# Optimization experiments

Measured on AMD Instinct MI355X. Metric: run time of the kernel, lower is better.

Reference implementation:

```python
import jax, jax.numpy as jnp
import numpy as np

N = 10000   # nodes
B = 32      # batch (hardcoded in source)
E = 40000   # edges per graph
H = 4       # attention heads
D = 10      # out_feats per head (hardcoded 10 in source)
T = 10      # GAT input feature size (hardcoded 10)
L = 2       # n_align_layers
NEG = 0.2   # LeakyReLU slope


def _leaky(z):
    return jnp.where(z >= 0, z, NEG * z)


def _ln(t):
    # LayerNorm((N,B,D), elementwise_affine=False): normalize over the whole tensor
    m = t.mean()
    v = ((t - m) ** 2).mean()
    return (t - m) * jax.lax.rsqrt(v + 1e-5)


def _gat(feat, fc_w, a_l, a_r, src, dst):
    # feat: (N,B,T); fc_w: (H*D,T); a_l,a_r: (H,D); src,dst: (E,)
    ft = jnp.einsum('nbf,of->nbo', feat, fc_w).reshape(N, B, H, D)
    el = jnp.einsum('nbhd,hd->nbh', ft, a_l)   # (N,B,H)
    er = jnp.einsum('nbhd,hd->nbh', ft, a_r)
    e = _leaky(el[src] + er[dst])              # (E,B,H)
    emax = jax.ops.segment_max(e, dst, num_segments=N)
    ee = jnp.exp(e - emax[dst])
    a = ee / jax.ops.segment_sum(ee, dst, num_segments=N)[dst]  # edge softmax per dst
    out = jax.ops.segment_sum(ft[src] * a[..., None], dst, num_segments=N)  # (N,B,H,D)
    return _leaky(out)  # activation = leaky_relu in source


def setup_inputs():
    key = jax.random.key(0)
    ks = iter(jax.random.split(key, 40))
    x = jax.random.normal(next(ks), (T, N, B, 3), dtype=jnp.float32)
    idx = lambda: jax.random.randint(next(ks), (E,), 0, N, dtype=jnp.int32)
    inp = {'x': x, 'ps_src': idx(), 'ps_dst': idx(), 'rl_src': idx(), 'rl_dst': idx()}
    def gat_params(name):
        inp[name + '_fc'] = jax.random.normal(next(ks), (L, H * D, T), dtype=jnp.float32) * 0.3
        inp[name + '_al'] = jax.random.normal(next(ks), (L, H, D), dtype=jnp.float32) * 0.3
        inp[name + '_ar'] = jax.random.normal(next(ks), (L, H, D), dtype=jnp.float32) * 0.3
    for nm in ('mu_p', 'sg_p', 'mu_r', 'sg_r'):
        gat_params(nm)
    inp['reg_mu_w'] = jax.random.normal(next(ks), (1, T), dtype=jnp.float32) * 0.3
    inp['reg_mu_b'] = jnp.zeros((1,), dtype=jnp.float32)
    inp['reg_sg_w'] = jax.random.normal(next(ks), (1, T), dtype=jnp.float32) * 0.3
    inp['reg_sg_b'] = jnp.zeros((1,), dtype=jnp.float32)
    return inp


def reference(x, mu_p_fc, mu_p_al, mu_p_ar, sg_p_fc, sg_p_al, sg_p_ar,
              mu_r_fc, mu_r_al, mu_r_ar, sg_r_fc, sg_r_al, sg_r_ar,
              reg_mu_w, reg_mu_b, reg_sg_w, reg_sg_b,
              ps_src, ps_dst, rl_src, rl_dst):
    # mode='align1' path of Net.forward
    h = jnp.transpose(x, (1, 2, 0, 3))[..., :3]  # (N,B,T,3)
    mu = h[..., 0]      # (N,B,T)
    sigma = h[..., 1]
    mu_r0, sg_r0 = mu, sigma
    # pseudo-graph alignment stack
    mu_p, sg_p = mu, sigma
    for i in range(L - 1):
        mu_p = _ln(_gat(mu_p, mu_p_fc[i], mu_p_al[i], mu_p_ar[i], ps_src, ps_dst).mean(-2))
        sg_p = _ln(_gat(sg_p, sg_p_fc[i], sg_p_al[i], sg_p_ar[i], ps_src, ps_dst).mean(-2))
        h_p = (mu_p + sg_p) / 2
        mu_p, sg_p = h_p, h_p
    # real-graph alignment stack
    mu_rl, sg_rl = mu, sigma
    for i in range(L - 1):
        mu_rl = _ln(_gat(mu_rl, mu_r_fc[i], mu_r_al[i], mu_r_ar[i], rl_src, rl_dst).mean(-2))
        sg_rl = _ln(_gat(sg_rl, sg_r_fc[i], sg_r_al[i], sg_r_ar[i], rl_src, rl_dst).mean(-2))
        h_rl = (mu_rl + sg_rl) / 2
        mu_rl, sg_rl = h_rl, h_rl
    mu_r = mu_r0 @ reg_mu_w.T + reg_mu_b                                        # (N,B,1)
    mu_pf = _gat(h_p, mu_p_fc[-1], mu_p_al[-1], mu_p_ar[-1], ps_src, ps_dst).mean(-2)
    mu_rf = _gat(h_rl, mu_r_fc[-1], mu_r_al[-1], mu_r_ar[-1], rl_src, rl_dst).mean(-2)
    sg_r = sg_r0 @ reg_sg_w.T + reg_sg_b
    sg_pf = _gat(h_p, sg_p_fc[-1], sg_p_al[-1], sg_p_ar[-1], ps_src, ps_dst).mean(-2)
    sg_rf = _gat(h_rl, sg_r_fc[-1], sg_r_al[-1], sg_r_ar[-1], rl_src, rl_dst).mean(-2)
    return ((mu_r + mu_pf + mu_rf) / 3, (sg_r + sg_pf + sg_rf) / 3)
```

## Files before the change

kernel.cpp:

```cpp
#include <hip/hip_runtime.h>


#define NN 10000
#define BB 32
#define EE 40000
#define HH 4
#define DD 10
#define TT 10
#define FS 12
#define MS 24
#define NEG 0.2f

#define NB   (NN*BB)
#define NBT  (NN*BB*TT)
#define NBF  (NN*BB*FS)
#define NBM  (NN*BB*MS)

__global__ void extract_kernel(const float* __restrict__ x,
                               const float* __restrict__ wmu, const float* __restrict__ bmu,
                               const float* __restrict__ wsg, const float* __restrict__ bsg,
                               float* __restrict__ ms,
                               float* __restrict__ regmu, float* __restrict__ regsg) {
    int i = blockIdx.x * blockDim.x + threadIdx.x;
    if (i >= NB) return;
    int n = i / BB, b = i % BB;
    float smu = 0.f, ssg = 0.f;
    float muv[TT], sgv[TT];
#pragma unroll
    for (int t = 0; t < TT; t++) {
        size_t xi = (((size_t)t * NN + n) * BB + b) * 3;
        float m = x[xi], s = x[xi + 1];
        muv[t] = m; sgv[t] = s;
        smu += m * wmu[t];
        ssg += s * wsg[t];
    }
#pragma unroll
    for (int t = 0; t < TT; t++) {
        ms[(size_t)i * MS + t]      = muv[t];
        ms[(size_t)i * MS + 12 + t] = sgv[t];
    }
    regmu[i] = smu + bmu[0];
    regsg[i] = ssg + bsg[0];
}

__global__ void deg2_kernel(const int* __restrict__ dst0, int* __restrict__ deg0,
                            const int* __restrict__ dst1, int* __restrict__ deg1) {
    int e = blockIdx.x * blockDim.x + threadIdx.x;
    const int* dst = blockIdx.y ? dst1 : dst0;
    int* deg       = blockIdx.y ? deg1 : deg0;
    if (e < EE) atomicAdd(&deg[dst[e]], 1);
}

__global__ void scan2_kernel(const int* __restrict__ deg0, int* __restrict__ off0,
                             const int* __restrict__ deg1, int* __restrict__ off1) {
    const int* __restrict__ deg = blockIdx.x ? deg1 : deg0;
    int* __restrict__ off       = blockIdx.x ? off1 : off0;
    __shared__ int sm[16];
    __shared__ int carry_s;
    int tid = threadIdx.x;
    int lane = tid & 63, wid = tid >> 6;
    if (tid == 0) { carry_s = 0; off[0] = 0; }
    __syncthreads();
    for (int base = 0; base < NN; base += 1024) {
        int i = base + tid;
        int v = (i < NN) ? deg[i] : 0;
        int x = v;
#pragma unroll
        for (int s = 1; s < 64; s <<= 1) {
            int t = __shfl_up(x, s, 64);
            if (lane >= s) x += t;
        }
        if (lane == 63) sm[wid] = x;
        __syncthreads();
        if (wid == 0) {
            int w = (lane < 16) ? sm[lane] : 0;
#pragma unroll
            for (int s = 1; s < 16; s <<= 1) {
                int t = __shfl_up(w, s, 64);
                if (lane >= s) w += t;
            }
            if (lane < 16) sm[lane] = w;
        }
        __syncthreads();
        int add = carry_s + ((wid > 0) ? sm[wid - 1] : 0);
        if (i < NN) off[i + 1] = add + x;
        int total = sm[15];
        __syncthreads();
        if (tid == 0) carry_s += total;
        __syncthreads();
    }
}

__global__ void fill2_kernel(const int* __restrict__ src0, const int* __restrict__ dst0,
                             const int* __restrict__ off0, int* __restrict__ cur0,
                             int* __restrict__ csr0,
                             const int* __restrict__ src1, const int* __restrict__ dst1,
                             const int* __restrict__ off1, int* __restrict__ cur1,
                             int* __restrict__ csr1) {
    int e = blockIdx.x * blockDim.x + threadIdx.x;
    const int* src = blockIdx.y ? src1 : src0;
    const int* dst = blockIdx.y ? dst1 : dst0;
    const int* off = blockIdx.y ? off1 : off0;
    int* cursor    = blockIdx.y ? cur1 : cur0;
    int* csr       = blockIdx.y ? csr1 : csr0;
    if (e < EE) {
        int d = dst[e];
        int p = atomicAdd(&cursor[d], 1);
        csr[off[d] + p] = src[e];
    }
}

__global__ void hist2_kernel(const int* __restrict__ deg0, const int* __restrict__ deg1,
                             int* __restrict__ hist) {
    __shared__ int lh[64];
    if (threadIdx.x < 64) lh[threadIdx.x] = 0;
    __syncthreads();
    int n = blockIdx.x * blockDim.x + threadIdx.x;
    int g = blockIdx.y;
    const int* deg = g ? deg1 : deg0;
    if (n < NN) {
        int d = deg[n];
        int bin = 63 - ((d < 63) ? d : 63);
        atomicAdd(&lh[bin], 1);
    }
    __syncthreads();
    if (threadIdx.x < 64 && lh[threadIdx.x])
        atomicAdd(&hist[g * 64 + threadIdx.x], lh[threadIdx.x]);
}

__global__ void binoff_kernel(const int* __restrict__ hist, int* __restrict__ boff) {
    int g = threadIdx.x >> 6, lane = threadIdx.x & 63;
    int v = hist[g * 64 + lane];
    int x = v;
#pragma unroll
    for (int s = 1; s < 64; s <<= 1) {
        int t = __shfl_up(x, s, 64);
        if (lane >= s) x += t;
    }
    boff[g * 64 + lane] = x - v;
}

__global__ void permfill2_kernel(const int* __restrict__ deg0, const int* __restrict__ deg1,
                                 const int* __restrict__ boff, int* __restrict__ bcur,
                                 int* __restrict__ perm0, int* __restrict__ perm1) {
    __shared__ int lh[64], lbase[64];
    if (threadIdx.x < 64) lh[threadIdx.x] = 0;
    __syncthreads();
    int n = blockIdx.x * blockDim.x + threadIdx.x;
    int g = blockIdx.y;
    const int* deg = g ? deg1 : deg0;
    int* perm      = g ? perm1 : perm0;
    int bin = 0, myp = 0;
    if (n < NN) {
        int d = deg[n];
        bin = 63 - ((d < 63) ? d : 63);
        myp = atomicAdd(&lh[bin], 1);
    }
    __syncthreads();
    if (threadIdx.x < 64) {
        int c = lh[threadIdx.x];
        lbase[threadIdx.x] = c ? atomicAdd(&bcur[g * 64 + threadIdx.x], c) : 0;
    }
    __syncthreads();
    if (n < NN) perm[boff[g * 64 + bin] + lbase[bin] + myp] = n;
}

__global__ void vpre_kernel(const float* __restrict__ fc0, const float* __restrict__ al0, const float* __restrict__ ar0,
                            const float* __restrict__ fc1, const float* __restrict__ al1, const float* __restrict__ ar1,
                            const float* __restrict__ fc2, const float* __restrict__ al2, const float* __restrict__ ar2,
                            const float* __restrict__ fc3, const float* __restrict__ al3, const float* __restrict__ ar3,
                            float* __restrict__ vbuf) {
    int j = threadIdx.x;
    if (j >= 320) return;
    int g = j / 40, r = j % 40;
    int h = r / 10, t = r % 10;
    int which = g & 3, layer = g >> 2;
    const float* fc; const float* al; const float* ar;
    if (which == 0)      { fc = fc0; al = al0; ar = ar0; }
    else if (which == 1) { fc = fc1; al = al1; ar = ar1; }
    else if (which == 2) { fc = fc2; al = al2; ar = ar2; }
    else                 { fc = fc3; al = al3; ar = ar3; }
    fc += layer * (HH * DD * TT);
    al += layer * (HH * DD);
    ar += layer * (HH * DD);
    float vl = 0.f, vr = 0.f;
#pragma unroll
    for (int d = 0; d < DD; d++) {
        float w = fc[(h * DD + d) * TT + t];
        vl += al[h * DD + d] * w;
        vr += ar[h * DD + d] * w;
    }
    vbuf[g * 80 + r] = vl;
    vbuf[g * 80 + 40 + r] = vr;
}

struct PairCfg {
    const float* f;
    const float* WA; const float* WB;
    const float* vA; const float* vB;
    const int* off; const int* csr; const int* perm;
    float* gA; float* gB;
    float* statsA; float* statsB;
};
struct PairCfg2 { PairCfg c[2]; };

#define LOAD_ROW(dst, q)                                        \
    {                                                           \
        float4 _r0 = *(const float4*)(q);                       \
        float4 _r1 = *(const float4*)((q) + 4);                 \
        float2 _r2 = *(const float2*)((q) + 8);                 \
        dst[0]=_r0.x; dst[1]=_r0.y; dst[2]=_r0.z; dst[3]=_r0.w; \
        dst[4]=_r1.x; dst[5]=_r1.y; dst[6]=_r1.z; dst[7]=_r1.w; \
        dst[8]=_r2.x; dst[9]=_r2.y;                             \
    }

__device__ __forceinline__ void eacc(const float (&fa)[TT], bool val,
                                     const float* __restrict__ v,
                                     const float (&er)[HH],
                                     float (&den)[HH], float (&acc)[HH][TT]) {
#pragma unroll
    for (int h = 0; h < HH; h++) {
        float e = 0.f;
#pragma unroll
        for (int t = 0; t < TT; t++) e += v[h * TT + t] * fa[t];
        float z = e + er[h];
        z = (z >= 0.f) ? z : NEG * z;
        float w = val ? __expf(z) : 0.f;
        den[h] += w;
#pragma unroll
        for (int t = 0; t < TT; t++) acc[h][t] += w * fa[t];
    }
}

template <bool DUALF, bool STATS>
__global__ void __launch_bounds__(256)
gatpair_kernel(PairCfg2 cfgs) {
    const PairCfg cfg = cfgs.c[blockIdx.y];
    __shared__ __align__(16) float sWA[HH * DD * 12];
    __shared__ __align__(16) float sWB[HH * DD * 12];
    for (int kk = threadIdx.x; kk < HH * DD * TT; kk += blockDim.x) {
        int r = kk / TT, t = kk - r * TT;
        sWA[r * 12 + t] = cfg.WA[kk];
        sWB[r * 12 + t] = cfg.WB[kk];
    }
    __syncthreads();

    const float* __restrict__ f   = cfg.f;
    const int*   __restrict__ csr = cfg.csr;
    const float* __restrict__ vA  = cfg.vA;
    const float* __restrict__ vB  = cfg.vB;
    const int LDR = DUALF ? MS : FS;

    int i = blockIdx.x * blockDim.x + threadIdx.x;
    float lsA = 0.f, lqA = 0.f, lsB = 0.f, lqB = 0.f;
    if (i < NB) {
        int b = i & 31;
        int slot = i >> 5;
        int n = cfg.perm[slot];
        int nb = n * BB + b;
        int s0 = cfg.off[n], s1 = cfg.off[n + 1];

        float erA[HH], erB[HH];
        {
            const float* p = f + (size_t)nb * LDR;
            float fsA[TT];
            LOAD_ROW(fsA, p);
            float fsB[TT];
            if (DUALF) { LOAD_ROW(fsB, p + 12); }
#pragma unroll
            for (int h = 0; h < HH; h++) {
                float ea = 0.f, eb = 0.f;
#pragma unroll
                for (int t = 0; t < TT; t++) {
                    ea += vA[HH * TT + h * TT + t] * fsA[t];
                    eb += vB[HH * TT + h * TT + t] * (DUALF ? fsB[t] : fsA[t]);
                }
                erA[h] = ea; erB[h] = eb;
            }
        }

        float accA[HH][TT], accB[HH][TT];
        float denA[HH], denB[HH];
#pragma unroll
        for (int h = 0; h < HH; h++) {
            denA[h] = 0.f; denB[h] = 0.f;
#pragma unroll
            for (int t = 0; t < TT; t++) { accA[h][t] = 0.f; accB[h][t] = 0.f; }
        }

        for (int k = s0; k < s1; k += 2) {
            int k1 = (k + 1 < s1) ? k + 1 : k;
            bool v1 = (k + 1 < s1);
            int e0 = csr[k], e1 = csr[k1];
            const float* q0 = f + (size_t)(e0 * BB + b) * LDR;
            const float* q1 = f + (size_t)(e1 * BB + b) * LDR;
            float a0[TT], a1[TT];
            LOAD_ROW(a0, q0);
            LOAD_ROW(a1, q1);
            if (DUALF) {
                float b0[TT], b1[TT];
                LOAD_ROW(b0, q0 + 12);
                LOAD_ROW(b1, q1 + 12);
                eacc(a0, true, vA, erA, denA, accA);
                eacc(b0, true, vB, erB, denB, accB);
                eacc(a1, v1,   vA, erA, denA, accA);
                eacc(b1, v1,   vB, erB, denB, accB);
            } else {
                eacc(a0, true, vA, erA, denA, accA);
                eacc(a0, true, vB, erB, denB, accB);
                eacc(a1, v1,   vA, erA, denA, accA);
                eacc(a1, v1,   vB, erB, denB, accB);
            }
        }

        bool nz = (s1 > s0);
        float* gpA = cfg.gA + (size_t)nb * DD;
        float* gpB = cfg.gB + (size_t)nb * DD;

#pragma unroll
        for (int g = 0; g < 2; g++) {
            const float (*acc)[TT] = g ? accB : accA;
            const float* den = g ? denB : denA;
            const float* sW  = g ? sWB : sWA;
            float* gp        = g ? gpB : gpA;
            float rd[HH];
#pragma unroll
            for (int h = 0; h < HH; h++) rd[h] = nz ? (1.0f / den[h]) : 0.f;
            float outv[DD];
#pragma unroll
            for (int d = 0; d < DD; d++) outv[d] = 0.f;
#pragma unroll
            for (int h = 0; h < HH; h++) {
#pragma unroll
                for (int d = 0; d < DD; d++) {
                    const float* wr = &sW[(h * DD + d) * 12];
                    float4 w0 = *(const float4*)wr;
                    float4 w1 = *(const float4*)(wr + 4);
                    float2 w2 = *(const float2*)(wr + 8);
                    float va = w0.x * acc[h][0] + w0.y * acc[h][1] + w0.z * acc[h][2] + w0.w * acc[h][3]
                             + w1.x * acc[h][4] + w1.y * acc[h][5] + w1.z * acc[h][6] + w1.w * acc[h][7]
                             + w2.x * acc[h][8] + w2.y * acc[h][9];
                    va *= rd[h];
                    va = (va >= 0.f) ? va : NEG * va;
                    outv[d] += va * 0.25f;
                }
            }
#pragma unroll
            for (int d = 0; d < DD; d += 2)
                *(float2*)(gp + d) = make_float2(outv[d], outv[d + 1]);
            if (STATS) {
                float s = 0.f, q = 0.f;
#pragma unroll
                for (int d = 0; d < DD; d++) { s += outv[d]; q += outv[d] * outv[d]; }
                if (g) { lsB = s; lqB = q; } else { lsA = s; lqA = q; }
            }
        }
    }
    if (STATS) {
#pragma unroll
        for (int o = 32; o > 0; o >>= 1) {
            lsA += __shfl_down(lsA, o, 64);
            lqA += __shfl_down(lqA, o, 64);
            lsB += __shfl_down(lsB, o, 64);
            lqB += __shfl_down(lqB, o, 64);
        }
        __shared__ float ss[4][4];
        int wid = threadIdx.x >> 6, lid = threadIdx.x & 63;
        if (lid == 0) { ss[wid][0] = lsA; ss[wid][1] = lqA; ss[wid][2] = lsB; ss[wid][3] = lqB; }
        __syncthreads();
        if (threadIdx.x == 0) {
            float a0 = 0.f, a1 = 0.f, a2 = 0.f, a3 = 0.f;
#pragma unroll
            for (int w = 0; w < 4; w++) { a0 += ss[w][0]; a1 += ss[w][1]; a2 += ss[w][2]; a3 += ss[w][3]; }
            atomicAdd(&cfg.statsA[0], a0);
            atomicAdd(&cfg.statsA[1], a1);
            atomicAdd(&cfg.statsB[0], a2);
            atomicAdd(&cfg.statsB[1], a3);
        }
    }
}

__global__ void lncomb2_kernel(const float* __restrict__ gA, const float* __restrict__ gB,
                               const float* __restrict__ gA2, const float* __restrict__ gB2,
                               const float* __restrict__ stats,
                               float* __restrict__ hp, float* __restrict__ hrl) {
    int i = blockIdx.x * blockDim.x + threadIdx.x;
    if (i >= NBT) return;
    const float* ga = blockIdx.y ? gA2 : gA;
    const float* gb = blockIdx.y ? gB2 : gB;
    const float* st = stats + (blockIdx.y ? 4 : 0);
    float* h        = blockIdx.y ? hrl : hp;
    const float M = (float)NBT;
    float ma = st[0] / M; float va = st[1] / M - ma * ma;
    float mb = st[2] / M; float vb = st[3] / M - mb * mb;
    float ra = rsqrtf(va + 1e-5f), rb = rsqrtf(vb + 1e-5f);
    int nb = i / DD, t = i - nb * DD;
    h[(size_t)nb * FS + t] = 0.5f * ((ga[i] - ma) * ra + (gb[i] - mb) * rb);
}

__global__ void outcomb2_kernel(const float* __restrict__ regmu, const float* __restrict__ regsg,
                                const float* __restrict__ gA, const float* __restrict__ gA2,
                                const float* __restrict__ gB, const float* __restrict__ gB2,
                                float* __restrict__ out) {
    int i = blockIdx.x * blockDim.x + threadIdx.x;
    if (i >= NBT) return;
    int nb = i / DD;
    if (blockIdx.y == 0) out[i]       = (regmu[nb] + gA[i] + gA2[i]) * (1.0f / 3.0f);
    else                 out[NBT + i] = (regsg[nb] + gB[i] + gB2[i]) * (1.0f / 3.0f);
}

extern "C" void kernel_launch(void* const* d_in, const int* in_sizes, int n_in,
                              void* d_out, int out_size, void* d_ws, size_t ws_size,
                              hipStream_t stream) {
    const float* x      = (const float*)d_in[0];
    const int* ps_src   = (const int*)d_in[1];
    const int* ps_dst   = (const int*)d_in[2];
    const int* rl_src   = (const int*)d_in[3];
    const int* rl_dst   = (const int*)d_in[4];
    const float* mu_p_fc = (const float*)d_in[5];
    const float* mu_p_al = (const float*)d_in[6];
    const float* mu_p_ar = (const float*)d_in[7];
    const float* sg_p_fc = (const float*)d_in[8];
    const float* sg_p_al = (const float*)d_in[9];
    const float* sg_p_ar = (const float*)d_in[10];
    const float* mu_r_fc = (const float*)d_in[11];
    const float* mu_r_al = (const float*)d_in[12];
    const float* mu_r_ar = (const float*)d_in[13];
    const float* sg_r_fc = (const float*)d_in[14];
    const float* sg_r_al = (const float*)d_in[15];
    const float* sg_r_ar = (const float*)d_in[16];
    const float* reg_mu_w = (const float*)d_in[17];
    const float* reg_mu_b = (const float*)d_in[18];
    const float* reg_sg_w = (const float*)d_in[19];
    const float* reg_sg_b = (const float*)d_in[20];

    float* out = (float*)d_out;

    float* fw = (float*)d_ws;
    float* ms    = fw;              fw += NBM;
    float* hp    = fw;              fw += NBF;
    float* hrl   = fw;              fw += NBF;
    float* gA    = fw;              fw += NBT;
    float* gB    = fw;              fw += NBT;
    float* gA2   = fw;              fw += NBT;
    float* gB2   = fw;              fw += NBT;
    float* regmu = fw;              fw += NB;
    float* regsg = fw;              fw += NB;
    float* vbuf  = fw;              fw += 8 * 80;
    int* iw = (int*)fw;
    int* ps_off = iw;               iw += NN + 1;
    int* rl_off = iw;               iw += NN + 1;
    int* ps_csr = iw;               iw += EE;
    int* rl_csr = iw;               iw += EE;
    int* perm_ps = iw;              iw += NN;
    int* perm_rl = iw;              iw += NN;
    int* boff   = iw;               iw += 128;
    int* deg_ps = iw;               iw += NN;
    int* cur_ps = iw;               iw += NN;
    int* deg_rl = iw;               iw += NN;
    int* cur_rl = iw;               iw += NN;
    int* hist   = iw;               iw += 128;
    int* bcur   = iw;               iw += 128;
    float* stats = (float*)iw;
    size_t zero_bytes = (size_t)(4 * NN + 256) * sizeof(int) + 8 * sizeof(float);
    hipMemsetAsync(deg_ps, 0, zero_bytes, stream);

    const int TPB = 256;
    const int GRID_NB  = (NB + TPB - 1) / TPB;
    const int GRID_NBT = (NBT + TPB - 1) / TPB;
    const int GRID_E   = (EE + TPB - 1) / TPB;
    const int GRID_N   = (NN + TPB - 1) / TPB;

    extract_kernel<<<GRID_NB, TPB, 0, stream>>>(x, reg_mu_w, reg_mu_b, reg_sg_w, reg_sg_b,
                                                ms, regmu, regsg);

    {
        dim3 g(GRID_E, 2, 1);
        dim3 gn(GRID_N, 2, 1);
        deg2_kernel<<<g, TPB, 0, stream>>>(ps_dst, deg_ps, rl_dst, deg_rl);
        scan2_kernel<<<2, 1024, 0, stream>>>(deg_ps, ps_off, deg_rl, rl_off);
        fill2_kernel<<<g, TPB, 0, stream>>>(ps_src, ps_dst, ps_off, cur_ps, ps_csr,
                                            rl_src, rl_dst, rl_off, cur_rl, rl_csr);
        hist2_kernel<<<gn, TPB, 0, stream>>>(deg_ps, deg_rl, hist);
        binoff_kernel<<<1, 128, 0, stream>>>(hist, boff);
        permfill2_kernel<<<gn, TPB, 0, stream>>>(deg_ps, deg_rl, boff, bcur, perm_ps, perm_rl);
    }

    vpre_kernel<<<1, 320, 0, stream>>>(mu_p_fc, mu_p_al, mu_p_ar,
                                       sg_p_fc, sg_p_al, sg_p_ar,
                                       mu_r_fc, mu_r_al, mu_r_ar,
                                       sg_r_fc, sg_r_al, sg_r_ar, vbuf);

    {
        PairCfg2 c;
        c.c[0] = { ms, mu_p_fc, sg_p_fc, vbuf + 0 * 80, vbuf + 1 * 80,
                   ps_off, ps_csr, perm_ps, gA,  gB,  stats + 0, stats + 2 };
        c.c[1] = { ms, mu_r_fc, sg_r_fc, vbuf + 2 * 80, vbuf + 3 * 80,
                   rl_off, rl_csr, perm_rl, gA2, gB2, stats + 4, stats + 6 };
        dim3 grid(GRID_NB, 2, 1);
        gatpair_kernel<true, true><<<grid, TPB, 0, stream>>>(c);
    }
    {
        dim3 g(GRID_NBT, 2, 1);
        lncomb2_kernel<<<g, TPB, 0, stream>>>(gA, gB, gA2, gB2, stats, hp, hrl);
    }

    {
        PairCfg2 c;
        c.c[0] = { hp,  mu_p_fc + 400, sg_p_fc + 400, vbuf + 4 * 80, vbuf + 5 * 80,
                   ps_off, ps_csr, perm_ps, gA,  gB,  nullptr, nullptr };
        c.c[1] = { hrl, mu_r_fc + 400, sg_r_fc + 400, vbuf + 6 * 80, vbuf + 7 * 80,
                   rl_off, rl_csr, perm_rl, gA2, gB2, nullptr, nullptr };
        dim3 grid(GRID_NB, 2, 1);
        gatpair_kernel<false, false><<<grid, TPB, 0, stream>>>(c);
    }

    {
        dim3 g(GRID_NBT, 2, 1);
        outcomb2_kernel<<<g, TPB, 0, stream>>>(regmu, regsg, gA, gA2, gB, gB2, out);
    }
}
```

Baseline: 413.2 us.

## Split GAT feature rows across half-wavefronts with transposed 6-wide layout

Features are stored in a transposed layout where each node-batch row is split into two 6-float halves, so one 64-lane wavefront handles one destination node across all 32 batches and both halves. Per-edge attention logits and the final projections are completed with cross-half shuffles. The paired A/B GAT kernel becomes a single-GAT kernel launched over four configs, and the neighbour loads are software-prefetched one edge ahead. The intent is to halve per-thread register state and raise occupancy and load parallelism, at the cost of extra shuffles and of reading the shared input rows separately for each GAT.

Result: slower. 556.1 us (+34.6%).

```diff
diff --git a/kernel.cpp b/kernel.cpp
--- a/kernel.cpp
+++ b/kernel.cpp
@@ -8,24 +8,22 @@
 #define DD 10
 #define TT 10
 #define FS 12
-#define MS 24
 #define NEG 0.2f
 
 #define NB   (NN*BB)
 #define NBT  (NN*BB*TT)
 #define NBF  (NN*BB*FS)
-#define NBM  (NN*BB*MS)
 
 __global__ void extract_kernel(const float* __restrict__ x,
                                const float* __restrict__ wmu, const float* __restrict__ bmu,
                                const float* __restrict__ wsg, const float* __restrict__ bsg,
-                               float* __restrict__ ms,
+                               float* __restrict__ muT, float* __restrict__ sgT,
                                float* __restrict__ regmu, float* __restrict__ regsg) {
     int i = blockIdx.x * blockDim.x + threadIdx.x;
     if (i >= NB) return;
     int n = i / BB, b = i % BB;
     float smu = 0.f, ssg = 0.f;
-    float muv[TT], sgv[TT];
+    float muv[FS], sgv[FS];
 #pragma unroll
     for (int t = 0; t < TT; t++) {
         size_t xi = (((size_t)t * NN + n) * BB + b) * 3;
@@ -34,10 +32,13 @@
         smu += m * wmu[t];
         ssg += s * wsg[t];
     }
-#pragma unroll
-    for (int t = 0; t < TT; t++) {
-        ms[(size_t)i * MS + t]      = muv[t];
-        ms[(size_t)i * MS + 12 + t] = sgv[t];
+    muv[10] = 0.f; muv[11] = 0.f; sgv[10] = 0.f; sgv[11] = 0.f;
+#pragma unroll
+    for (int t = 0; t < FS; t++) {
+        int th = t / 6, j = t - th * 6;
+        size_t di = ((size_t)(n * 2 + th) * BB + b) * 6 + j;
+        muT[di] = muv[t];
+        sgT[di] = sgv[t];
     }
     regmu[i] = smu + bmu[0];
     regsg[i] = ssg + bsg[0];
@@ -194,188 +195,160 @@
     vbuf[g * 80 + 40 + r] = vr;
 }
 
-struct PairCfg {
+struct QCfg {
     const float* f;
-    const float* WA; const float* WB;
-    const float* vA; const float* vB;
+    const float* W;
+    const float* v;
     const int* off; const int* csr; const int* perm;
-    float* gA; float* gB;
-    float* statsA; float* statsB;
+    float* g; float* stats;
 };
-struct PairCfg2 { PairCfg c[2]; };
-
-#define LOAD_ROW(dst, q)                                        \
-    {                                                           \
-        float4 _r0 = *(const float4*)(q);                       \
-        float4 _r1 = *(const float4*)((q) + 4);                 \
-        float2 _r2 = *(const float2*)((q) + 8);                 \
-        dst[0]=_r0.x; dst[1]=_r0.y; dst[2]=_r0.z; dst[3]=_r0.w; \
-        dst[4]=_r1.x; dst[5]=_r1.y; dst[6]=_r1.z; dst[7]=_r1.w; \
-        dst[8]=_r2.x; dst[9]=_r2.y;                             \
-    }
-
-__device__ __forceinline__ void eacc(const float (&fa)[TT], bool val,
-                                     const float* __restrict__ v,
-                                     const float (&er)[HH],
-                                     float (&den)[HH], float (&acc)[HH][TT]) {
-#pragma unroll
-    for (int h = 0; h < HH; h++) {
-        float e = 0.f;
-#pragma unroll
-        for (int t = 0; t < TT; t++) e += v[h * TT + t] * fa[t];
-        float z = e + er[h];
-        z = (z >= 0.f) ? z : NEG * z;
-        float w = val ? __expf(z) : 0.f;
-        den[h] += w;
-#pragma unroll
-        for (int t = 0; t < TT; t++) acc[h][t] += w * fa[t];
-    }
-}
-
-template <bool DUALF, bool STATS>
+struct QCfg4 { QCfg c[4]; };
+
+template <bool STATS>
 __global__ void __launch_bounds__(256)
-gatpair_kernel(PairCfg2 cfgs) {
-    const PairCfg cfg = cfgs.c[blockIdx.y];
-    __shared__ __align__(16) float sWA[HH * DD * 12];
-    __shared__ __align__(16) float sWB[HH * DD * 12];
-    for (int kk = threadIdx.x; kk < HH * DD * TT; kk += blockDim.x) {
-        int r = kk / TT, t = kk - r * TT;
-        sWA[r * 12 + t] = cfg.WA[kk];
-        sWB[r * 12 + t] = cfg.WB[kk];
-    }
-    __syncthreads();
-
-    const float* __restrict__ f   = cfg.f;
-    const int*   __restrict__ csr = cfg.csr;
-    const float* __restrict__ vA  = cfg.vA;
-    const float* __restrict__ vB  = cfg.vB;
-    const int LDR = DUALF ? MS : FS;
-
-    int i = blockIdx.x * blockDim.x + threadIdx.x;
-    float lsA = 0.f, lqA = 0.f, lsB = 0.f, lqB = 0.f;
-    if (i < NB) {
-        int b = i & 31;
-        int slot = i >> 5;
+gatq_kernel(QCfg4 cfgs) {
+    const QCfg cfg = cfgs.c[blockIdx.y];
+    __shared__ __align__(16) float sW[HH * DD * 12];
+    __shared__ float svp[2 * HH * 12];
+    for (int kk = threadIdx.x; kk < HH * DD * 12; kk += blockDim.x) {
+        int r = kk / 12, t = kk - r * 12;
+        sW[kk] = (t < TT) ? cfg.W[r * TT + t] : 0.f;
+    }
+    if (threadIdx.x < 2 * HH * 12) {
+        int s = threadIdx.x / 48, r = threadIdx.x % 48;
+        int h = r / 12, t = r % 12;
+        svp[threadIdx.x] = (t < TT) ? cfg.v[s * 40 + h * TT + t] : 0.f;
+    }
+    __syncthreads();
+
+    int wid = threadIdx.x >> 6, lane = threadIdx.x & 63;
+    int th = lane >> 5, b = lane & 31;
+    int slot = blockIdx.x * 4 + wid;
+    float lsum = 0.f, lsq = 0.f;
+    if (slot < NN) {
         int n = cfg.perm[slot];
-        int nb = n * BB + b;
         int s0 = cfg.off[n], s1 = cfg.off[n + 1];
-
-        float erA[HH], erB[HH];
+        const float* __restrict__ f = cfg.f;
+        const int*   __restrict__ csr = cfg.csr;
+
+        float vl[HH][6];
+#pragma unroll
+        for (int h = 0; h < HH; h++)
+#pragma unroll
+            for (int j = 0; j < 6; j++) vl[h][j] = svp[h * 12 + th * 6 + j];
+
+        float er[HH];
         {
-            const float* p = f + (size_t)nb * LDR;
-            float fsA[TT];
-            LOAD_ROW(fsA, p);
-            float fsB[TT];
-            if (DUALF) { LOAD_ROW(fsB, p + 12); }
+            const float* p = f + ((size_t)n * 64 + lane) * 6;
+            float2 a = *(const float2*)p;
+            float2 c = *(const float2*)(p + 2);
+            float2 d = *(const float2*)(p + 4);
+            float fs[6] = {a.x, a.y, c.x, c.y, d.x, d.y};
 #pragma unroll
             for (int h = 0; h < HH; h++) {
-                float ea = 0.f, eb = 0.f;
-#pragma unroll
-                for (int t = 0; t < TT; t++) {
-                    ea += vA[HH * TT + h * TT + t] * fsA[t];
-                    eb += vB[HH * TT + h * TT + t] * (DUALF ? fsB[t] : fsA[t]);
-                }
-                erA[h] = ea; erB[h] = eb;
-            }
-        }
-
-        float accA[HH][TT], accB[HH][TT];
-        float denA[HH], denB[HH];
+                float e = 0.f;
+#pragma unroll
+                for (int j = 0; j < 6; j++) e += svp[48 + h * 12 + th * 6 + j] * fs[j];
+                e += __shfl_xor(e, 32, 64);
+                er[h] = e;
+            }
+        }
+
+        float acc[HH][6];
+        float den[HH];
 #pragma unroll
         for (int h = 0; h < HH; h++) {
-            denA[h] = 0.f; denB[h] = 0.f;
-#pragma unroll
-            for (int t = 0; t < TT; t++) { accA[h][t] = 0.f; accB[h][t] = 0.f; }
-        }
-
-        for (int k = s0; k < s1; k += 2) {
-            int k1 = (k + 1 < s1) ? k + 1 : k;
-            bool v1 = (k + 1 < s1);
-            int e0 = csr[k], e1 = csr[k1];
-            const float* q0 = f + (size_t)(e0 * BB + b) * LDR;
-            const float* q1 = f + (size_t)(e1 * BB + b) * LDR;
-            float a0[TT], a1[TT];
-            LOAD_ROW(a0, q0);
-            LOAD_ROW(a1, q1);
-            if (DUALF) {
-                float b0[TT], b1[TT];
-                LOAD_ROW(b0, q0 + 12);
-                LOAD_ROW(b1, q1 + 12);
-                eacc(a0, true, vA, erA, denA, accA);
-                eacc(b0, true, vB, erB, denB, accB);
-                eacc(a1, v1,   vA, erA, denA, accA);
-                eacc(b1, v1,   vB, erB, denB, accB);
-            } else {
-                eacc(a0, true, vA, erA, denA, accA);
-                eacc(a0, true, vB, erB, denB, accB);
-                eacc(a1, v1,   vA, erA, denA, accA);
-                eacc(a1, v1,   vB, erB, denB, accB);
-            }
+            den[h] = 0.f;
+#pragma unroll
+            for (int j = 0; j < 6; j++) acc[h][j] = 0.f;
+        }
+
+        int e2 = 0;
+        float2 n0, n1, n2;
+        if (s0 < s1) {
+            int e1 = csr[s0];
+            const float* q = f + ((size_t)e1 * 64 + lane) * 6;
+            n0 = *(const float2*)q; n1 = *(const float2*)(q + 2); n2 = *(const float2*)(q + 4);
+            e2 = (s0 + 1 < s1) ? csr[s0 + 1] : e1;
+        }
+        for (int k = s0; k < s1; k++) {
+            float cur[6] = {n0.x, n0.y, n1.x, n1.y, n2.x, n2.y};
+            if (k + 1 < s1) {
+                const float* q = f + ((size_t)e2 * 64 + lane) * 6;
+                n0 = *(const float2*)q; n1 = *(const float2*)(q + 2); n2 = *(const float2*)(q + 4);
+            }
+            if (k + 2 < s1) e2 = csr[k + 2];
+            float w[HH];
+#pragma unroll
+            for (int h = 0; h < HH; h++) {
+                float el = 0.f;
+#pragma unroll
+                for (int j = 0; j < 6; j++) el += vl[h][j] * cur[j];
+                el += __shfl_xor(el, 32, 64);
+                float z = el + er[h];
+                z = (z >= 0.f) ? z : NEG * z;
+                float ww = __expf(z);
+                w[h] = ww;
+                den[h] += ww;
+            }
+#pragma unroll
+            for (int h = 0; h < HH; h++)
+#pragma unroll
+                for (int j = 0; j < 6; j++) acc[h][j] += w[h] * cur[j];
         }
 
         bool nz = (s1 > s0);
-        float* gpA = cfg.gA + (size_t)nb * DD;
-        float* gpB = cfg.gB + (size_t)nb * DD;
-
-#pragma unroll
-        for (int g = 0; g < 2; g++) {
-            const float (*acc)[TT] = g ? accB : accA;
-            const float* den = g ? denB : denA;
-            const float* sW  = g ? sWB : sWA;
-            float* gp        = g ? gpB : gpA;
-            float rd[HH];
-#pragma unroll
-            for (int h = 0; h < HH; h++) rd[h] = nz ? (1.0f / den[h]) : 0.f;
-            float outv[DD];
-#pragma unroll
-            for (int d = 0; d < DD; d++) outv[d] = 0.f;
-#pragma unroll
-            for (int h = 0; h < HH; h++) {
-#pragma unroll
-                for (int d = 0; d < DD; d++) {
-                    const float* wr = &sW[(h * DD + d) * 12];
-                    float4 w0 = *(const float4*)wr;
-                    float4 w1 = *(const float4*)(wr + 4);
-                    float2 w2 = *(const float2*)(wr + 8);
-                    float va = w0.x * acc[h][0] + w0.y * acc[h][1] + w0.z * acc[h][2] + w0.w * acc[h][3]
-                             + w1.x * acc[h][4] + w1.y * acc[h][5] + w1.z * acc[h][6] + w1.w * acc[h][7]
-                             + w2.x * acc[h][8] + w2.y * acc[h][9];
-                    va *= rd[h];
-                    va = (va >= 0.f) ? va : NEG * va;
-                    outv[d] += va * 0.25f;
-                }
-            }
+        float outv[DD];
+#pragma unroll
+        for (int d = 0; d < DD; d++) outv[d] = 0.f;
+#pragma unroll
+        for (int h = 0; h < HH; h++) {
+            float rd = nz ? (1.0f / den[h]) : 0.f;
+            float yh[DD];
+#pragma unroll
+            for (int d = 0; d < DD; d++) {
+                const float2* wp = (const float2*)&sW[(h * DD + d) * 12 + th * 6];
+                float2 w0 = wp[0], w1 = wp[1], w2 = wp[2];
+                yh[d] = w0.x * acc[h][0] + w0.y * acc[h][1]
+                      + w1.x * acc[h][2] + w1.y * acc[h][3]
+                      + w2.x * acc[h][4] + w2.y * acc[h][5];
+            }
+#pragma unroll
+            for (int d = 0; d < DD; d++) {
+                float y = yh[d] + __shfl_xor(yh[d], 32, 64);
+                y *= rd;
+                y = (y >= 0.f) ? y : NEG * y;
+                outv[d] += 0.25f * y;
+            }
+        }
+
+        if (th == 0) {
+            float* gp = cfg.g + ((size_t)n * BB + b) * DD;
 #pragma unroll
             for (int d = 0; d < DD; d += 2)
                 *(float2*)(gp + d) = make_float2(outv[d], outv[d + 1]);
             if (STATS) {
-                float s = 0.f, q = 0.f;
-#pragma unroll
-                for (int d = 0; d < DD; d++) { s += outv[d]; q += outv[d] * outv[d]; }
-                if (g) { lsB = s; lqB = q; } else { lsA = s; lqA = q; }
+#pragma unroll
+                for (int d = 0; d < DD; d++) { lsum += outv[d]; lsq += outv[d] * outv[d]; }
             }
         }
     }
     if (STATS) {
 #pragma unroll
         for (int o = 32; o > 0; o >>= 1) {
-            lsA += __shfl_down(lsA, o, 64);
-            lqA += __shfl_down(lqA, o, 64);
-            lsB += __shfl_down(lsB, o, 64);
-            lqB += __shfl_down(lqB, o, 64);
-        }
-        __shared__ float ss[4][4];
-        int wid = threadIdx.x >> 6, lid = threadIdx.x & 63;
-        if (lid == 0) { ss[wid][0] = lsA; ss[wid][1] = lqA; ss[wid][2] = lsB; ss[wid][3] = lqB; }
+            lsum += __shfl_down(lsum, o, 64);
+            lsq  += __shfl_down(lsq, o, 64);
+        }
+        __shared__ float ss[4][2];
+        int lid = threadIdx.x & 63;
+        if (lid == 0) { ss[threadIdx.x >> 6][0] = lsum; ss[threadIdx.x >> 6][1] = lsq; }
         __syncthreads();
         if (threadIdx.x == 0) {
-            float a0 = 0.f, a1 = 0.f, a2 = 0.f, a3 = 0.f;
-#pragma unroll
-            for (int w = 0; w < 4; w++) { a0 += ss[w][0]; a1 += ss[w][1]; a2 += ss[w][2]; a3 += ss[w][3]; }
-            atomicAdd(&cfg.statsA[0], a0);
-            atomicAdd(&cfg.statsA[1], a1);
-            atomicAdd(&cfg.statsB[0], a2);
-            atomicAdd(&cfg.statsB[1], a3);
+            float a0 = 0.f, a1 = 0.f;
+#pragma unroll
+            for (int w = 0; w < 4; w++) { a0 += ss[w][0]; a1 += ss[w][1]; }
+            atomicAdd(&cfg.stats[0], a0);
+            atomicAdd(&cfg.stats[1], a1);
         }
     }
 }
@@ -385,17 +358,24 @@
                                const float* __restrict__ stats,
                                float* __restrict__ hp, float* __restrict__ hrl) {
     int i = blockIdx.x * blockDim.x + threadIdx.x;
-    if (i >= NBT) return;
+    if (i >= NB * FS) return;
     const float* ga = blockIdx.y ? gA2 : gA;
     const float* gb = blockIdx.y ? gB2 : gB;
     const float* st = stats + (blockIdx.y ? 4 : 0);
     float* h        = blockIdx.y ? hrl : hp;
-    const float M = (float)NBT;
-    float ma = st[0] / M; float va = st[1] / M - ma * ma;
-    float mb = st[2] / M; float vb = st[3] / M - mb * mb;
-    float ra = rsqrtf(va + 1e-5f), rb = rsqrtf(vb + 1e-5f);
-    int nb = i / DD, t = i - nb * DD;
-    h[(size_t)nb * FS + t] = 0.5f * ((ga[i] - ma) * ra + (gb[i] - mb) * rb);
+    int nb = i / FS, t = i - nb * FS;
+    float val = 0.f;
+    if (t < TT) {
+        const float M = (float)NBT;
+        float ma = st[0] / M; float va = st[1] / M - ma * ma;
+        float mb = st[2] / M; float vb = st[3] / M - mb * mb;
+        float ra = rsqrtf(va + 1e-5f), rb = rsqrtf(vb + 1e-5f);
+        float a = ga[(size_t)nb * DD + t], bb = gb[(size_t)nb * DD + t];
+        val = 0.5f * ((a - ma) * ra + (bb - mb) * rb);
+    }
+    int n = nb >> 5, b = nb & 31;
+    int tth = t / 6, j = t - tth * 6;
+    h[((size_t)(n * 2 + tth) * BB + b) * 6 + j] = val;
 }
 
 __global__ void outcomb2_kernel(const float* __restrict__ regmu, const float* __restrict__ regsg,
@@ -437,9 +417,10 @@
     float* out = (float*)d_out;
 
     float* fw = (float*)d_ws;
-    float* ms    = fw;              fw += NBM;
-    float* hp    = fw;              fw += NBF;
-    float* hrl   = fw;              fw += NBF;
+    float* muT   = fw;              fw += NBF;
+    float* sgT   = fw;              fw += NBF;
+    float* hpT   = fw;              fw += NBF;
+    float* hrlT  = fw;              fw += NBF;
     float* gA    = fw;              fw += NBT;
     float* gB    = fw;              fw += NBT;
     float* gA2   = fw;              fw += NBT;
@@ -468,11 +449,13 @@
     const int TPB = 256;
     const int GRID_NB  = (NB + TPB - 1) / TPB;
     const int GRID_NBT = (NBT + TPB - 1) / TPB;
+    const int GRID_NBF = (NB * FS + TPB - 1) / TPB;
     const int GRID_E   = (EE + TPB - 1) / TPB;
     const int GRID_N   = (NN + TPB - 1) / TPB;
+    const int GRID_Q   = (NN + 3) / 4;
 
     extract_kernel<<<GRID_NB, TPB, 0, stream>>>(x, reg_mu_w, reg_mu_b, reg_sg_w, reg_sg_b,
-                                                ms, regmu, regsg);
+                                                muT, sgT, regmu, regsg);
 
     {
         dim3 g(GRID_E, 2, 1);
@@ -492,27 +475,27 @@
                                        sg_r_fc, sg_r_al, sg_r_ar, vbuf);
 
     {
-        PairCfg2 c;
-        c.c[0] = { ms, mu_p_fc, sg_p_fc, vbuf + 0 * 80, vbuf + 1 * 80,
-                   ps_off, ps_csr, perm_ps, gA,  gB,  stats + 0, stats + 2 };
-        c.c[1] = { ms, mu_r_fc, sg_r_fc, vbuf + 2 * 80, vbuf + 3 * 80,
-                   rl_off, rl_csr, perm_rl, gA2, gB2, stats + 4, stats + 6 };
-        dim3 grid(GRID_NB, 2, 1);
-        gatpair_kernel<true, true><<<grid, TPB, 0, stream>>>(c);
+        QCfg4 c;
+        c.c[0] = { muT, mu_p_fc,       vbuf + 0 * 80, ps_off, ps_csr, perm_ps, gA,  stats + 0 };
+        c.c[1] = { sgT, sg_p_fc,       vbuf + 1 * 80, ps_off, ps_csr, perm_ps, gB,  stats + 2 };
+        c.c[2] = { muT, mu_r_fc,       vbuf + 2 * 80, rl_off, rl_csr, perm_rl, gA2, stats + 4 };
+        c.c[3] = { sgT, sg_r_fc,       vbuf + 3 * 80, rl_off, rl_csr, perm_rl, gB2, stats + 6 };
+        dim3 grid(GRID_Q, 4, 1);
+        gatq_kernel<true><<<grid, TPB, 0, stream>>>(c);
     }
     {
-        dim3 g(GRID_NBT, 2, 1);
-        lncomb2_kernel<<<g, TPB, 0, stream>>>(gA, gB, gA2, gB2, stats, hp, hrl);
+        dim3 g(GRID_NBF, 2, 1);
+        lncomb2_kernel<<<g, TPB, 0, stream>>>(gA, gB, gA2, gB2, stats, hpT, hrlT);
     }
 
     {
-        PairCfg2 c;
-        c.c[0] = { hp,  mu_p_fc + 400, sg_p_fc + 400, vbuf + 4 * 80, vbuf + 5 * 80,
-                   ps_off, ps_csr, perm_ps, gA,  gB,  nullptr, nullptr };
-        c.c[1] = { hrl, mu_r_fc + 400, sg_r_fc + 400, vbuf + 6 * 80, vbuf + 7 * 80,
-                   rl_off, rl_csr, perm_rl, gA2, gB2, nullptr, nullptr };
-        dim3 grid(GRID_NB, 2, 1);
-        gatpair_kernel<false, false><<<grid, TPB, 0, stream>>>(c);
+        QCfg4 c;
+        c.c[0] = { hpT,  mu_p_fc + 400, vbuf + 4 * 80, ps_off, ps_csr, perm_ps, gA,  nullptr };
+        c.c[1] = { hpT,  sg_p_fc + 400, vbuf + 5 * 80, ps_off, ps_csr, perm_ps, gB,  nullptr };
+        c.c[2] = { hrlT, mu_r_fc + 400, vbuf + 6 * 80, rl_off, rl_csr, perm_rl, gA2, nullptr };
+        c.c[3] = { hrlT, sg_r_fc + 400, vbuf + 7 * 80, rl_off, rl_csr, perm_rl, gB2, nullptr };
+        dim3 grid(GRID_Q, 4, 1);
+        gatq_kernel<false><<<grid, TPB, 0, stream>>>(c);
     }
 
     {
```

## Store gathered GAT features in fp16 and widen neighbor gather unroll

Applied to the files above, without the earlier changes.

Gathered node features (inputs and intermediate LN outputs) are stored as packed fp16 rows (48/32 bytes instead of 96/48) and unpacked to fp32 in the GAT kernel. This halves the bytes moved by random neighbor gathers. The edge loop is unrolled to four neighbors to keep more loads in flight. The thread-to-(node,batch) mapping now gives each wave 32 nodes with 2 batches each, not 1 node with 32 batches. The fp16 storage lowers precision of intermediates, and the new mapping changes coalescing and load balance across waves.

Result: slower. 423.0 us (+2.4%).

```diff
diff --git a/kernel.cpp b/kernel.cpp
--- a/kernel.cpp
+++ b/kernel.cpp
@@ -1,4 +1,5 @@
 #include <hip/hip_runtime.h>
+#include <hip/hip_fp16.h>
 
 
 #define NN 10000
@@ -7,19 +8,38 @@
 #define HH 4
 #define DD 10
 #define TT 10
-#define FS 12
-#define MS 24
 #define NEG 0.2f
 
 #define NB   (NN*BB)
 #define NBT  (NN*BB*TT)
-#define NBF  (NN*BB*FS)
-#define NBM  (NN*BB*MS)
+#define BSUB 2
+#define NGRP (NN*BSUB)
+
+
+__device__ __forceinline__ float2 cvt2(unsigned u) {
+    return __half22float2(*reinterpret_cast<const __half2*>(&u));
+}
+__device__ __forceinline__ void unpA(const uint4& u0, const uint4& u1, float (&fa)[10]) {
+    float2 t;
+    t = cvt2(u0.x); fa[0] = t.x; fa[1] = t.y;
+    t = cvt2(u0.y); fa[2] = t.x; fa[3] = t.y;
+    t = cvt2(u0.z); fa[4] = t.x; fa[5] = t.y;
+    t = cvt2(u0.w); fa[6] = t.x; fa[7] = t.y;
+    t = cvt2(u1.x); fa[8] = t.x; fa[9] = t.y;
+}
+__device__ __forceinline__ void unpB(const uint4& u1, const uint4& u2, float (&fb)[10]) {
+    float2 t;
+    t = cvt2(u1.z); fb[0] = t.x; fb[1] = t.y;
+    t = cvt2(u1.w); fb[2] = t.x; fb[3] = t.y;
+    t = cvt2(u2.x); fb[4] = t.x; fb[5] = t.y;
+    t = cvt2(u2.y); fb[6] = t.x; fb[7] = t.y;
+    t = cvt2(u2.z); fb[8] = t.x; fb[9] = t.y;
+}
 
 __global__ void extract_kernel(const float* __restrict__ x,
                                const float* __restrict__ wmu, const float* __restrict__ bmu,
                                const float* __restrict__ wsg, const float* __restrict__ bsg,
-                               float* __restrict__ ms,
+                               __half* __restrict__ msH,
                                float* __restrict__ regmu, float* __restrict__ regsg) {
     int i = blockIdx.x * blockDim.x + threadIdx.x;
     if (i >= NB) return;
@@ -34,11 +54,19 @@
         smu += m * wmu[t];
         ssg += s * wsg[t];
     }
-#pragma unroll
-    for (int t = 0; t < TT; t++) {
-        ms[(size_t)i * MS + t]      = muv[t];
-        ms[(size_t)i * MS + 12 + t] = sgv[t];
-    }
+    __half2* dst = (__half2*)(msH + (size_t)i * 24);
+    dst[0] = __floats2half2_rn(muv[0], muv[1]);
+    dst[1] = __floats2half2_rn(muv[2], muv[3]);
+    dst[2] = __floats2half2_rn(muv[4], muv[5]);
+    dst[3] = __floats2half2_rn(muv[6], muv[7]);
+    dst[4] = __floats2half2_rn(muv[8], muv[9]);
+    dst[5] = __floats2half2_rn(0.f, 0.f);
+    dst[6] = __floats2half2_rn(sgv[0], sgv[1]);
+    dst[7] = __floats2half2_rn(sgv[2], sgv[3]);
+    dst[8] = __floats2half2_rn(sgv[4], sgv[5]);
+    dst[9] = __floats2half2_rn(sgv[6], sgv[7]);
+    dst[10] = __floats2half2_rn(sgv[8], sgv[9]);
+    dst[11] = __floats2half2_rn(0.f, 0.f);
     regmu[i] = smu + bmu[0];
     regsg[i] = ssg + bsg[0];
 }
@@ -195,7 +223,7 @@
 }
 
 struct PairCfg {
-    const float* f;
+    const __half* f;
     const float* WA; const float* WB;
     const float* vA; const float* vB;
     const int* off; const int* csr; const int* perm;
@@ -203,16 +231,6 @@
     float* statsA; float* statsB;
 };
 struct PairCfg2 { PairCfg c[2]; };
-
-#define LOAD_ROW(dst, q)                                        \
-    {                                                           \
-        float4 _r0 = *(const float4*)(q);                       \
-        float4 _r1 = *(const float4*)((q) + 4);                 \
-        float2 _r2 = *(const float2*)((q) + 8);                 \
-        dst[0]=_r0.x; dst[1]=_r0.y; dst[2]=_r0.z; dst[3]=_r0.w; \
-        dst[4]=_r1.x; dst[5]=_r1.y; dst[6]=_r1.z; dst[7]=_r1.w; \
-        dst[8]=_r2.x; dst[9]=_r2.y;                             \
-    }
 
 __device__ __forceinline__ void eacc(const float (&fa)[TT], bool val,
                                      const float* __restrict__ v,
@@ -245,35 +263,43 @@
     }
     __syncthreads();
 
-    const float* __restrict__ f   = cfg.f;
+    const __half* __restrict__ f  = cfg.f;
     const int*   __restrict__ csr = cfg.csr;
     const float* __restrict__ vA  = cfg.vA;
     const float* __restrict__ vB  = cfg.vB;
-    const int LDR = DUALF ? MS : FS;
+    const int LDR = DUALF ? 24 : 16;
 
     int i = blockIdx.x * blockDim.x + threadIdx.x;
     float lsA = 0.f, lqA = 0.f, lsB = 0.f, lqB = 0.f;
     if (i < NB) {
-        int b = i & 31;
-        int slot = i >> 5;
+        int bgrp = i / NGRP;
+        int r = i - bgrp * NGRP;
+        int slot = r >> 1;
+        int b = (bgrp << 1) | (r & 1);
         int n = cfg.perm[slot];
         int nb = n * BB + b;
         int s0 = cfg.off[n], s1 = cfg.off[n + 1];
 
         float erA[HH], erB[HH];
         {
-            const float* p = f + (size_t)nb * LDR;
-            float fsA[TT];
-            LOAD_ROW(fsA, p);
-            float fsB[TT];
-            if (DUALF) { LOAD_ROW(fsB, p + 12); }
+            const uint4* p = (const uint4*)(f + (size_t)nb * LDR);
+            float fsA[TT], fsB[TT];
+            if (DUALF) {
+                uint4 u0 = p[0], u1 = p[1], u2 = p[2];
+                unpA(u0, u1, fsA); unpB(u1, u2, fsB);
+            } else {
+                uint4 u0 = p[0], u1 = p[1];
+                unpA(u0, u1, fsA);
+#pragma unroll
+                for (int t = 0; t < TT; t++) fsB[t] = fsA[t];
+            }
 #pragma unroll
             for (int h = 0; h < HH; h++) {
                 float ea = 0.f, eb = 0.f;
 #pragma unroll
                 for (int t = 0; t < TT; t++) {
                     ea += vA[HH * TT + h * TT + t] * fsA[t];
-                    eb += vB[HH * TT + h * TT + t] * (DUALF ? fsB[t] : fsA[t]);
+                    eb += vB[HH * TT + h * TT + t] * fsB[t];
                 }
                 erA[h] = ea; erB[h] = eb;
             }
@@ -288,28 +314,44 @@
             for (int t = 0; t < TT; t++) { accA[h][t] = 0.f; accB[h][t] = 0.f; }
         }
 
-        for (int k = s0; k < s1; k += 2) {
-            int k1 = (k + 1 < s1) ? k + 1 : k;
-            bool v1 = (k + 1 < s1);
-            int e0 = csr[k], e1 = csr[k1];
-            const float* q0 = f + (size_t)(e0 * BB + b) * LDR;
-            const float* q1 = f + (size_t)(e1 * BB + b) * LDR;
-            float a0[TT], a1[TT];
-            LOAD_ROW(a0, q0);
-            LOAD_ROW(a1, q1);
+        for (int k = s0; k < s1; k += 4) {
+            int k1 = (k + 1 < s1) ? k + 1 : s0;
+            int k2 = (k + 2 < s1) ? k + 2 : s0;
+            int k3 = (k + 3 < s1) ? k + 3 : s0;
+            bool v1 = (k + 1 < s1), v2 = (k + 2 < s1), v3 = (k + 3 < s1);
+            int e0 = csr[k], e1 = csr[k1], e2 = csr[k2], e3 = csr[k3];
+            const uint4* q0 = (const uint4*)(f + (size_t)(e0 * BB + b) * LDR);
+            const uint4* q1 = (const uint4*)(f + (size_t)(e1 * BB + b) * LDR);
+            const uint4* q2 = (const uint4*)(f + (size_t)(e2 * BB + b) * LDR);
+            const uint4* q3 = (const uint4*)(f + (size_t)(e3 * BB + b) * LDR);
             if (DUALF) {
-                float b0[TT], b1[TT];
-                LOAD_ROW(b0, q0 + 12);
-                LOAD_ROW(b1, q1 + 12);
-                eacc(a0, true, vA, erA, denA, accA);
-                eacc(b0, true, vB, erB, denB, accB);
-                eacc(a1, v1,   vA, erA, denA, accA);
-                eacc(b1, v1,   vB, erB, denB, accB);
+                uint4 a0 = q0[0], a1 = q0[1], a2 = q0[2];
+                uint4 b0 = q1[0], b1 = q1[1], b2 = q1[2];
+                uint4 c0 = q2[0], c1 = q2[1], c2 = q2[2];
+                uint4 d0 = q3[0], d1 = q3[1], d2 = q3[2];
+                float fa[TT], fb[TT];
+                unpA(a0, a1, fa); unpB(a1, a2, fb);
+                eacc(fa, true, vA, erA, denA, accA); eacc(fb, true, vB, erB, denB, accB);
+                unpA(b0, b1, fa); unpB(b1, b2, fb);
+                eacc(fa, v1, vA, erA, denA, accA);   eacc(fb, v1, vB, erB, denB, accB);
+                unpA(c0, c1, fa); unpB(c1, c2, fb);
+                eacc(fa, v2, vA, erA, denA, accA);   eacc(fb, v2, vB, erB, denB, accB);
+                unpA(d0, d1, fa); unpB(d1, d2, fb);
+                eacc(fa, v3, vA, erA, denA, accA);   eacc(fb, v3, vB, erB, denB, accB);
             } else {
-                eacc(a0, true, vA, erA, denA, accA);
-                eacc(a0, true, vB, erB, denB, accB);
-                eacc(a1, v1,   vA, erA, denA, accA);
-                eacc(a1, v1,   vB, erB, denB, accB);
+                uint4 a0 = q0[0], a1 = q0[1];
+                uint4 b0 = q1[0], b1 = q1[1];
+                uint4 c0 = q2[0], c1 = q2[1];
+                uint4 d0 = q3[0], d1 = q3[1];
+                float fa[TT];
+                unpA(a0, a1, fa);
+                eacc(fa, true, vA, erA, denA, accA); eacc(fa, true, vB, erB, denB, accB);
+                unpA(b0, b1, fa);
+                eacc(fa, v1, vA, erA, denA, accA);   eacc(fa, v1, vB, erB, denB, accB);
+                unpA(c0, c1, fa);
+                eacc(fa, v2, vA, erA, denA, accA);   eacc(fa, v2, vB, erB, denB, accB);
+                unpA(d0, d1, fa);
+                eacc(fa, v3, vA, erA, denA, accA);   eacc(fa, v3, vB, erB, denB, accB);
             }
         }
 
@@ -383,19 +425,25 @@
 __global__ void lncomb2_kernel(const float* __restrict__ gA, const float* __restrict__ gB,
                                const float* __restrict__ gA2, const float* __restrict__ gB2,
                                const float* __restrict__ stats,
-                               float* __restrict__ hp, float* __restrict__ hrl) {
+                               __half* __restrict__ hp, __half* __restrict__ hrl) {
     int i = blockIdx.x * blockDim.x + threadIdx.x;
-    if (i >= NBT) return;
+    if (i >= NB * 8) return;
     const float* ga = blockIdx.y ? gA2 : gA;
     const float* gb = blockIdx.y ? gB2 : gB;
     const float* st = stats + (blockIdx.y ? 4 : 0);
-    float* h        = blockIdx.y ? hrl : hp;
-    const float M = (float)NBT;
-    float ma = st[0] / M; float va = st[1] / M - ma * ma;
-    float mb = st[2] / M; float vb = st[3] / M - mb * mb;
-    float ra = rsqrtf(va + 1e-5f), rb = rsqrtf(vb + 1e-5f);
-    int nb = i / DD, t = i - nb * DD;
-    h[(size_t)nb * FS + t] = 0.5f * ((ga[i] - ma) * ra + (gb[i] - mb) * rb);
+    __half2* h      = (__half2*)(blockIdx.y ? hrl : hp);
+    int nb = i >> 3, t2 = i & 7;
+    float v0 = 0.f, v1 = 0.f;
+    if (t2 < 5) {
+        const float M = (float)NBT;
+        float ma = st[0] / M; float va = st[1] / M - ma * ma;
+        float mb = st[2] / M; float vb = st[3] / M - mb * mb;
+        float ra = rsqrtf(va + 1e-5f), rb = rsqrtf(vb + 1e-5f);
+        size_t base = (size_t)nb * DD + t2 * 2;
+        v0 = 0.5f * ((ga[base] - ma) * ra + (gb[base] - mb) * rb);
+        v1 = 0.5f * ((ga[base + 1] - ma) * ra + (gb[base + 1] - mb) * rb);
+    }
+    h[(size_t)nb * 8 + t2] = __floats2half2_rn(v0, v1);
 }
 
 __global__ void outcomb2_kernel(const float* __restrict__ regmu, const float* __restrict__ regsg,
@@ -437,9 +485,9 @@
     float* out = (float*)d_out;
 
     float* fw = (float*)d_ws;
-    float* ms    = fw;              fw += NBM;
-    float* hp    = fw;              fw += NBF;
-    float* hrl   = fw;              fw += NBF;
+    __half* msH  = (__half*)fw;     fw += NB * 12;
+    __half* hpH  = (__half*)fw;     fw += NB * 8;
+    __half* hrlH = (__half*)fw;     fw += NB * 8;
     float* gA    = fw;              fw += NBT;
     float* gB    = fw;              fw += NBT;
     float* gA2   = fw;              fw += NBT;
@@ -468,11 +516,12 @@
     const int TPB = 256;
     const int GRID_NB  = (NB + TPB - 1) / TPB;
     const int GRID_NBT = (NBT + TPB - 1) / TPB;
+    const int GRID_LN  = (NB * 8 + TPB - 1) / TPB;
     const int GRID_E   = (EE + TPB - 1) / TPB;
     const int GRID_N   = (NN + TPB - 1) / TPB;
 
     extract_kernel<<<GRID_NB, TPB, 0, stream>>>(x, reg_mu_w, reg_mu_b, reg_sg_w, reg_sg_b,
-                                                ms, regmu, regsg);
+                                                msH, regmu, regsg);
 
     {
         dim3 g(GRID_E, 2, 1);
@@ -493,23 +542,23 @@
 
     {
         PairCfg2 c;
-        c.c[0] = { ms, mu_p_fc, sg_p_fc, vbuf + 0 * 80, vbuf + 1 * 80,
+        c.c[0] = { msH, mu_p_fc, sg_p_fc, vbuf + 0 * 80, vbuf + 1 * 80,
                    ps_off, ps_csr, perm_ps, gA,  gB,  stats + 0, stats + 2 };
-        c.c[1] = { ms, mu_r_fc, sg_r_fc, vbuf + 2 * 80, vbuf + 3 * 80,
+        c.c[1] = { msH, mu_r_fc, sg_r_fc, vbuf + 2 * 80, vbuf + 3 * 80,
                    rl_off, rl_csr, perm_rl, gA2, gB2, stats + 4, stats + 6 };
         dim3 grid(GRID_NB, 2, 1);
         gatpair_kernel<true, true><<<grid, TPB, 0, stream>>>(c);
     }
     {
-        dim3 g(GRID_NBT, 2, 1);
-        lncomb2_kernel<<<g, TPB, 0, stream>>>(gA, gB, gA2, gB2, stats, hp, hrl);
+        dim3 g(GRID_LN, 2, 1);
+        lncomb2_kernel<<<g, TPB, 0, stream>>>(gA, gB, gA2, gB2, stats, hpH, hrlH);
     }
 
     {
         PairCfg2 c;
-        c.c[0] = { hp,  mu_p_fc + 400, sg_p_fc + 400, vbuf + 4 * 80, vbuf + 5 * 80,
+        c.c[0] = { hpH,  mu_p_fc + 400, sg_p_fc + 400, vbuf + 4 * 80, vbuf + 5 * 80,
                    ps_off, ps_csr, perm_ps, gA,  gB,  nullptr, nullptr };
-        c.c[1] = { hrl, mu_r_fc + 400, sg_r_fc + 400, vbuf + 6 * 80, vbuf + 7 * 80,
+        c.c[1] = { hrlH, mu_r_fc + 400, sg_r_fc + 400, vbuf + 6 * 80, vbuf + 7 * 80,
                    rl_off, rl_csr, perm_rl, gA2, gB2, nullptr, nullptr };
         dim3 grid(GRID_NB, 2, 1);
         gatpair_kernel<false, false><<<grid, TPB, 0, stream>>>(c);
```
